# Kernel optimization log

Hardware: AMD Instinct MI355X
Metric: run time of the kernel (lower is better)

Reference implementation:

```python
import jax, jax.numpy as jnp
import numpy as np

C = 1000      # num_classes
U = 10        # proxies_per_class
D = 512       # feature_dim
B = 4096      # batch
ALPHA = 32.0
DELTA = 0.1


def _l2norm(x, axis=-1):
    return x / jnp.linalg.norm(x, axis=axis, keepdims=True).clip(1e-12)


def setup_inputs() -> dict:
    key = jax.random.key(0)
    k1, k2, k3 = jax.random.split(key, 3)
    features = jax.random.normal(k1, (B, D), dtype=jnp.float32)
    labels = jax.random.randint(k2, (B,), 0, C)
    # proxies are initialized to row-normalized gaussians (as in __init__)
    proxies = _l2norm(jax.random.normal(k3, (C * U, D), dtype=jnp.float32))
    return {"features": features, "labels": labels, "proxies": proxies}


def reference(features, labels, proxies):
    # proxy_class_ids: [C*U], class id of each proxy
    class_ids = jnp.repeat(jnp.arange(C), U)

    x = _l2norm(features)          # [B, D]
    p = _l2norm(proxies)           # [P, D], P = C*U
    sim = x @ p.T                  # [B, P]

    # ---- infer_logits, agg='soft', tau=1 ----
    s = sim.reshape(B, C, U)       # per-class proxy similarities
    w = jax.nn.softmax(s, axis=2)
    logits = jnp.sum(w * s, axis=2)  # [B, C], tau=1 so no extra scaling

    # ---- _compute_proxy_loss (Proxy-Anchor) ----
    sim_t = sim.T                                         # [P, B]
    pos_mask = labels[None, :] == class_ids[:, None]      # [P, B]
    neg_inf = jnp.finfo(jnp.float32).min
    z_pos = jnp.where(pos_mask, -ALPHA * (sim_t - DELTA), neg_inf)
    z_neg = jnp.where(pos_mask, neg_inf, ALPHA * (sim_t + DELTA))
    lse_pos = jax.nn.logsumexp(z_pos, axis=1)             # [P]
    lse_neg = jax.nn.logsumexp(z_neg, axis=1)             # [P]
    pos_term = jax.nn.softplus(lse_pos)
    neg_term = jax.nn.softplus(lse_neg)
    has_pos = pos_mask.any(axis=1)
    pos_loss = jnp.where(has_pos, pos_term, 0.0).sum() / jnp.maximum(
        has_pos.sum(), 1).astype(jnp.float32)
    neg_loss = neg_term.mean()
    proxy_loss = pos_loss + neg_loss

    return logits, proxy_loss
```

## Files before the change

### kernel.cpp

```cpp
#include <hip/hip_runtime.h>
#include <hip/hip_bf16.h>

#define C_CLS   1000
#define U_PX    10
#define D_DIM   512
#define B_BATCH 4096
#define P_PX    (C_CLS * U_PX)
#define ALPHA_F 32.0f
#define DELTA_F 0.1f

#define BM 256
#define BN 80
#define BK 64
#define SIMP 84

#define A_OFF   0
#define B_OFF   32768
#define SMEM_SZ 43008

#define ZERO_DBL (2 * P_PX + 4)
#define FIN_BLK  ((P_PX + 255) / 256)

typedef __attribute__((ext_vector_type(8))) short bf16x8;
typedef __attribute__((ext_vector_type(4))) float f32x4;

typedef __attribute__((address_space(1))) const void gv_t;
typedef __attribute__((address_space(3))) void lv_t;

__device__ __forceinline__ void gload_lds16(const void* g, void* lds) {
    __builtin_amdgcn_global_load_lds((gv_t*)g, (lv_t*)lds, 16, 0, 0);
}

__device__ __forceinline__ unsigned int f2bf(float f) {
    union { float f; unsigned u; } c; c.f = f;
    unsigned u = c.u;
    return (u + 0x7FFF + ((u >> 16) & 1)) >> 16;
}

__global__ __launch_bounds__(256) void norm_rows_kernel(const float* __restrict__ feat,
                                                        const float* __restrict__ prox,
                                                        unsigned int* __restrict__ xout,
                                                        unsigned int* __restrict__ pout,
                                                        double* __restrict__ zbase) {
    const int zidx = blockIdx.x * 256 + threadIdx.x;
    if (zidx < ZERO_DBL) zbase[zidx] = 0.0;

    const int wid  = threadIdx.x >> 6;
    const int lane = threadIdx.x & 63;
    int row = blockIdx.x * 4 + wid;
    const float* in;
    unsigned int* out;
    if (row < B_BATCH) { in = feat + (size_t)row * D_DIM;   out = xout + (size_t)row * (D_DIM / 2); }
    else { row -= B_BATCH; in = prox + (size_t)row * D_DIM; out = pout + (size_t)row * (D_DIM / 2); }
    const float4 v0 = reinterpret_cast<const float4*>(in)[lane * 2];
    const float4 v1 = reinterpret_cast<const float4*>(in)[lane * 2 + 1];
    float ss = v0.x*v0.x + v0.y*v0.y + v0.z*v0.z + v0.w*v0.w
             + v1.x*v1.x + v1.y*v1.y + v1.z*v1.z + v1.w*v1.w;
    #pragma unroll
    for (int off = 1; off < 64; off <<= 1) ss += __shfl_xor(ss, off, 64);
    const float inv = 1.0f / fmaxf(sqrtf(ss), 1e-12f);
    uint4 o;
    o.x = f2bf(v0.x * inv) | (f2bf(v0.y * inv) << 16);
    o.y = f2bf(v0.z * inv) | (f2bf(v0.w * inv) << 16);
    o.z = f2bf(v1.x * inv) | (f2bf(v1.y * inv) << 16);
    o.w = f2bf(v1.z * inv) | (f2bf(v1.w * inv) << 16);
    *reinterpret_cast<uint4*>(out + lane * 4) = o;
}

__global__ __launch_bounds__(256, 3) void fused_gemm_kernel(
    const unsigned short* __restrict__ xbf,
    const unsigned short* __restrict__ pbf,
    const int*            __restrict__ labels,
    float*                __restrict__ logits,
    double*               __restrict__ pos_sum,
    double*               __restrict__ neg_sum)
{
    __shared__ __align__(16) char smem[SMEM_SZ];
    __shared__ int lab_lds[BM];

    const int t    = threadIdx.x;
    const int m0   = blockIdx.x * BM;
    const int n0   = blockIdx.y * BN;
    const int wid  = t >> 6;
    const int lane = t & 63;
    const int l15  = lane & 15;
    const int kgrp = lane >> 4;

    if (t < BM) lab_lds[t] = labels[m0 + t];

    const int srow = lane >> 3;
    const int scol = (lane & 7) ^ srow;

    const int koff0 = ((kgrp    ) ^ (l15 & 7)) << 4;
    const int koff1 = ((kgrp + 4) ^ (l15 & 7)) << 4;

    f32x4 acc[4][5];
    #pragma unroll
    for (int m = 0; m < 4; ++m)
        #pragma unroll
        for (int n = 0; n < 5; ++n) acc[m][n] = (f32x4){0.f, 0.f, 0.f, 0.f};

    for (int ks = 0; ks < D_DIM / BK; ++ks) {
        const int kbase = ks * BK;
        #pragma unroll
        for (int c = wid; c < 32; c += 4)
            gload_lds16(xbf + (size_t)(m0 + c * 8 + srow) * D_DIM + kbase + scol * 8,
                        smem + A_OFF + c * 1024);
        for (int c = wid; c < 10; c += 4)
            gload_lds16(pbf + (size_t)(n0 + c * 8 + srow) * D_DIM + kbase + scol * 8,
                        smem + B_OFF + c * 1024);
        __syncthreads();
        __builtin_amdgcn_s_setprio(1);
        #pragma unroll
        for (int kk8 = 0; kk8 < 2; ++kk8) {
            const int koff = kk8 ? koff1 : koff0;
            bf16x8 b[5];
            #pragma unroll
            for (int n = 0; n < 5; ++n)
                b[n] = *reinterpret_cast<const bf16x8*>(smem + B_OFF + (n * 16 + l15) * 128 + koff);
            #pragma unroll
            for (int m = 0; m < 4; ++m) {
                const bf16x8 a = *reinterpret_cast<const bf16x8*>(
                    smem + A_OFF + (wid * 64 + m * 16 + l15) * 128 + koff);
                #pragma unroll
                for (int n = 0; n < 5; ++n)
                    acc[m][n] = __builtin_amdgcn_mfma_f32_16x16x32_bf16(a, b[n], acc[m][n], 0, 0, 0);
            }
        }
        __builtin_amdgcn_s_setprio(0);
        __syncthreads();
    }

    {
        int labv[16];
        #pragma unroll
        for (int m = 0; m < 4; ++m)
            #pragma unroll
            for (int r = 0; r < 4; ++r)
                labv[m * 4 + r] = lab_lds[wid * 64 + m * 16 + kgrp * 4 + r];
        #pragma unroll
        for (int n = 0; n < 5; ++n) {
            const int col = n * 16 + l15;
            const int cls = (n0 + col) / U_PX;
            float pos = 0.f, neg = 0.f;
            #pragma unroll
            for (int m = 0; m < 4; ++m)
                #pragma unroll
                for (int r = 0; r < 4; ++r) {
                    const float s = acc[m][n][r];
                    const bool isp = (labv[m * 4 + r] == cls);
                    const float e = __expf(isp ? (-ALPHA_F * (s - DELTA_F))
                                               : ( ALPHA_F * (s + DELTA_F)));
                    if (isp) pos += e; else neg += e;
                }
            pos += __shfl_xor(pos, 16, 64); pos += __shfl_xor(pos, 32, 64);
            neg += __shfl_xor(neg, 16, 64); neg += __shfl_xor(neg, 32, 64);
            if (lane < 16) {
                atomicAdd(&neg_sum[n0 + col], (double)neg);
                if (pos != 0.f) atomicAdd(&pos_sum[n0 + col], (double)pos);
            }
        }
    }

    float* simw = reinterpret_cast<float*>(smem) + wid * (16 * SIMP);
    #pragma unroll
    for (int m = 0; m < 4; ++m) {
        #pragma unroll
        for (int n = 0; n < 5; ++n)
            #pragma unroll
            for (int r = 0; r < 4; ++r)
                simw[(kgrp * 4 + r) * SIMP + n * 16 + l15] = acc[m][n][r];
        #pragma unroll
        for (int it = 0; it < 2; ++it) {
            const int j   = lane + it * 64;
            const int r   = j >> 3;
            const int c   = j & 7;
            const float* s = simw + r * SIMP + c * U_PX;
            float wsum = 0.f, wssum = 0.f;
            #pragma unroll
            for (int u = 0; u < U_PX; ++u) {
                const float sv = s[u];
                const float e = __expf(sv);
                wsum += e; wssum += e * sv;
            }
            logits[(size_t)(m0 + wid * 64 + m * 16 + r) * C_CLS + (n0 / U_PX + c)] = wssum / wsum;
        }
        __builtin_amdgcn_s_waitcnt(0);
    }
}

__global__ __launch_bounds__(256) void finalize_kernel(
    const double* __restrict__ pos_sum,
    const double* __restrict__ neg_sum,
    double*       __restrict__ accum,
    float*        __restrict__ out_loss)
{
    const int p = blockIdx.x * 256 + threadIdx.x;
    double pv = 0.0, nv = 0.0;
    int c = 0;
    if (p < P_PX) {
        nv = log1p(neg_sum[p]);
        const double ps = pos_sum[p];
        if (ps != 0.0) { pv = log1p(ps); c = 1; }
    }
    #pragma unroll
    for (int off = 1; off < 64; off <<= 1) {
        pv += __shfl_xor(pv, off, 64);
        nv += __shfl_xor(nv, off, 64);
        c  += __shfl_xor(c,  off, 64);
    }
    if ((threadIdx.x & 63) == 0) {
        atomicAdd(&accum[0], pv);
        atomicAdd(&accum[1], nv);
        atomicAdd((int*)(accum + 2), c);
    }
    __syncthreads();
    __threadfence();
    if (threadIdx.x == 0) {
        const unsigned prev = atomicAdd((unsigned*)(accum + 3), 1u);
        if (prev == FIN_BLK - 1) {
            const double a0 = atomicAdd(&accum[0], 0.0);
            const double a1 = atomicAdd(&accum[1], 0.0);
            const int   cnt = atomicAdd((int*)(accum + 2), 0);
            out_loss[0] = (float)(a0 / (double)max(cnt, 1) + a1 / (double)P_PX);
        }
    }
}

extern "C" void kernel_launch(void* const* d_in, const int* in_sizes, int n_in,
                              void* d_out, int out_size, void* d_ws, size_t ws_size,
                              hipStream_t stream) {
    const float* features = (const float*)d_in[0];
    const int*   labels   = (const int*)d_in[1];
    const float* proxies  = (const float*)d_in[2];
    float* out = (float*)d_out;

    char* ws = (char*)d_ws;
    unsigned short* xbf = (unsigned short*)ws;
    unsigned short* pbf = (unsigned short*)(ws + (size_t)B_BATCH * D_DIM * 2);
    double* pos_sum = (double*)(ws + (size_t)(B_BATCH + P_PX) * D_DIM * 2);
    double* neg_sum = pos_sum + P_PX;
    double* accum   = neg_sum + P_PX;

    norm_rows_kernel<<<(B_BATCH + P_PX) / 4, 256, 0, stream>>>(
        features, proxies, (unsigned int*)xbf, (unsigned int*)pbf, pos_sum);

    fused_gemm_kernel<<<dim3(B_BATCH / BM, P_PX / BN), 256, 0, stream>>>(
        xbf, pbf, labels, out, pos_sum, neg_sum);

    finalize_kernel<<<FIN_BLK, 256, 0, stream>>>(pos_sum, neg_sum, accum,
                                                 out + (size_t)B_BATCH * C_CLS);
}
```

Baseline: 87.21 us.

## Double-buffer proxy tile and prefetch next K-slice during MFMA compute

Splits the B (proxy) LDS region into two buffers so the next K-slice of proxies is issued via global_load_lds before the current MFMA loop runs. The A (feature) slice is reloaded right after compute. Each wave loads only the A rows it reads itself, so no cross-wave barrier is needed before overwriting A. This cuts the loop to one vmcnt wait plus barrier per iteration instead of two __syncthreads. LDS use grows by one B tile, and the A load latency stays largely exposed.

```diff
diff --git a/kernel.cpp b/kernel.cpp
--- a/kernel.cpp
+++ b/kernel.cpp
@@ -13,10 +13,12 @@
 #define BN 80
 #define BK 64
 #define SIMP 84
-
-#define A_OFF   0
-#define B_OFF   32768
-#define SMEM_SZ 43008
+#define NKS (D_DIM / BK)
+
+#define A_OFF    0
+#define B_OFF    32768
+#define B_STRIDE 10240
+#define SMEM_SZ  (32768 + 2 * B_STRIDE)
 
 #define ZERO_DBL (2 * P_PX + 4)
 #define FIN_BLK  ((P_PX + 255) / 256)
@@ -100,16 +102,33 @@
         #pragma unroll
         for (int n = 0; n < 5; ++n) acc[m][n] = (f32x4){0.f, 0.f, 0.f, 0.f};
 
-    for (int ks = 0; ks < D_DIM / BK; ++ks) {
-        const int kbase = ks * BK;
-        #pragma unroll
-        for (int c = wid; c < 32; c += 4)
-            gload_lds16(xbf + (size_t)(m0 + c * 8 + srow) * D_DIM + kbase + scol * 8,
-                        smem + A_OFF + c * 1024);
-        for (int c = wid; c < 10; c += 4)
-            gload_lds16(pbf + (size_t)(n0 + c * 8 + srow) * D_DIM + kbase + scol * 8,
-                        smem + B_OFF + c * 1024);
-        __syncthreads();
+    #define STAGE_A(ks_)                                                                \
+        do {                                                                            \
+            const int kb_ = (ks_) * BK;                                                 \
+            _Pragma("unroll")                                                           \
+            for (int i = 0; i < 8; ++i) {                                               \
+                const int c_ = wid * 8 + i;                                             \
+                gload_lds16(xbf + (size_t)(m0 + c_ * 8 + srow) * D_DIM + kb_ + scol * 8,\
+                            smem + A_OFF + c_ * 1024);                                  \
+            }                                                                           \
+        } while (0)
+
+    #define STAGE_B(ks_, buf_)                                                          \
+        do {                                                                            \
+            const int kb_ = (ks_) * BK;                                                 \
+            char* bb_ = smem + B_OFF + (buf_) * B_STRIDE;                               \
+            for (int c_ = wid; c_ < 10; c_ += 4)                                        \
+                gload_lds16(pbf + (size_t)(n0 + c_ * 8 + srow) * D_DIM + kb_ + scol * 8,\
+                            bb_ + c_ * 1024);                                           \
+        } while (0)
+
+    STAGE_B(0, 0);
+    STAGE_A(0);
+    asm volatile("s_waitcnt vmcnt(0)\n\ts_barrier" ::: "memory");
+
+    for (int ks = 0; ks < NKS; ++ks) {
+        const char* bbase = smem + B_OFF + (ks & 1) * B_STRIDE;
+        if (ks < NKS - 1) STAGE_B(ks + 1, (ks + 1) & 1);
         __builtin_amdgcn_s_setprio(1);
         #pragma unroll
         for (int kk8 = 0; kk8 < 2; ++kk8) {
@@ -117,7 +136,7 @@
             bf16x8 b[5];
             #pragma unroll
             for (int n = 0; n < 5; ++n)
-                b[n] = *reinterpret_cast<const bf16x8*>(smem + B_OFF + (n * 16 + l15) * 128 + koff);
+                b[n] = *reinterpret_cast<const bf16x8*>(bbase + (n * 16 + l15) * 128 + koff);
             #pragma unroll
             for (int m = 0; m < 4; ++m) {
                 const bf16x8 a = *reinterpret_cast<const bf16x8*>(
@@ -128,7 +147,10 @@
             }
         }
         __builtin_amdgcn_s_setprio(0);
-        __syncthreads();
+        asm volatile("s_waitcnt lgkmcnt(0)" ::: "memory");
+        __builtin_amdgcn_sched_barrier(0);
+        if (ks < NKS - 1) STAGE_A(ks + 1);
+        asm volatile("s_waitcnt vmcnt(0)\n\ts_barrier" ::: "memory");
     }
 
     {
```

Result: slower. 97.40 us (+11.7%).
